# Optimization experiments

Hardware: AMD Instinct MI355X
Metric: run time of the kernel (lower is better)

## Reference

```python
import jax, jax.numpy as jnp
import numpy as np

B, C, H, W = 2, 32, 128, 128
P = 32                      # encoder patch size (== decoder_out_feat_size_final_linear -> empty up_tail)
D = 512                     # encoder dim == decoder dim (enc_to_dec = Identity)
HEADS, DHEAD = 8, 64
ENC_DEPTH = 4
FLIN, CUP = 32, 4
DI, DS, K, DTR, OUTCH = 32, 8, 4, 2, 20   # SS2D dims (c_in=32 hardcoded in module)


def _ln(x, g, b):
    m = x.mean(-1, keepdims=True)
    v = ((x - m) ** 2).mean(-1, keepdims=True)
    return (x - m) / jnp.sqrt(v + 1e-5) * g + b


def _attn(x, g, b, wqkv, wo, bo):
    Bb, N, _ = x.shape
    qkv = _ln(x, g, b) @ wqkv
    q, k, v = jnp.split(qkv, 3, axis=-1)
    sp = lambda t: t.reshape(Bb, N, HEADS, DHEAD).transpose(0, 2, 1, 3)
    q, k, v = sp(q), sp(k), sp(v)
    a = jax.nn.softmax(jnp.einsum('bhnd,bhmd->bhnm', q, k) * (DHEAD ** -0.5), axis=-1)
    o = jnp.einsum('bhnm,bhmd->bhnd', a, v).transpose(0, 2, 1, 3).reshape(Bb, N, HEADS * DHEAD)
    return o @ wo + bo


def _ff(x, g, b, w1, b1, w2, b2):
    return jax.nn.gelu(_ln(x, g, b) @ w1 + b1, approximate=False) @ w2 + b2


def _conv(x, w, b, groups=1):
    y = jax.lax.conv_general_dilated(x, w, (1, 1), 'SAME',
        dimension_numbers=('NCHW', 'OIHW', 'NCHW'), feature_group_count=groups)
    return y + b[None, :, None, None]


def _fft2c(x):
    x = jnp.fft.ifftshift(x, axes=(-2, -1))
    x = jnp.fft.fft2(x, axes=(-2, -1), norm='ortho')
    return jnp.fft.fftshift(x, axes=(-2, -1))


def _ifft2c(x):
    x = jnp.fft.ifftshift(x, axes=(-2, -1))
    x = jnp.fft.ifft2(x, axes=(-2, -1), norm='ortho')
    return jnp.fft.fftshift(x, axes=(-2, -1))


def setup_inputs():
    key = jax.random.key(0)
    it = iter(jax.random.split(key, 80))
    nk = lambda: next(it)
    rn = lambda shape, s=0.02: jax.random.normal(nk(), shape, jnp.float32) * s
    nh, nw = H // P, W // P
    N = nh * nw
    pd = P * P * C
    inp = {}
    inp['in_imgs'] = jax.random.normal(nk(), (B, C, H, W), jnp.float32)
    inp['in_ksp'] = rn((B, C, H, W), 0.01)
    inp['mask'] = (jax.random.uniform(nk(), (B, 1, H, W)) < 0.3).astype(jnp.float32)
    s = jax.random.normal(nk(), (B, C, H, W), jnp.float32)
    sc = s[:, 0::2] + 1j * s[:, 1::2]
    sc = sc / jnp.sqrt(jnp.sum(jnp.abs(sc) ** 2, axis=1, keepdims=True) + 1e-8)
    inp['sens'] = jnp.stack([sc.real, sc.imag], axis=2).reshape(B, C, H, W)
    # patch embedding: LayerNorm(pd) -> Linear(pd, D) -> LayerNorm(D)
    inp['pe_ln1_g'] = jnp.ones((pd,)); inp['pe_ln1_b'] = jnp.zeros((pd,))
    inp['pe_w'] = rn((pd, D)); inp['pe_b'] = jnp.zeros((D,))
    inp['pe_ln2_g'] = jnp.ones((D,)); inp['pe_ln2_b'] = jnp.zeros((D,))
    inp['pos_emb'] = rn((1, N, D))
    dep = ENC_DEPTH
    inp['enc_aln_g'] = jnp.ones((dep, D)); inp['enc_aln_b'] = jnp.zeros((dep, D))
    inp['enc_wqkv'] = rn((dep, D, 3 * HEADS * DHEAD)); inp['enc_wo'] = rn((dep, HEADS * DHEAD, D)); inp['enc_bo'] = jnp.zeros((dep, D))
    inp['enc_fln_g'] = jnp.ones((dep, D)); inp['enc_fln_b'] = jnp.zeros((dep, D))
    inp['enc_w1'] = rn((dep, D, 2048)); inp['enc_b1'] = jnp.zeros((dep, 2048))
    inp['enc_w2'] = rn((dep, 2048, D)); inp['enc_b2'] = jnp.zeros((dep, D))
    inp['enc_ng'] = jnp.ones((D,)); inp['enc_nb'] = jnp.zeros((D,))
    inp['dec_pos'] = rn((N, D))
    inp['dec_aln_g'] = jnp.ones((D,)); inp['dec_aln_b'] = jnp.zeros((D,))
    inp['dec_wqkv'] = rn((D, 3 * HEADS * DHEAD)); inp['dec_wo'] = rn((HEADS * DHEAD, D)); inp['dec_bo'] = jnp.zeros((D,))
    inp['dec_fln_g'] = jnp.ones((D,)); inp['dec_fln_b'] = jnp.zeros((D,))
    inp['dec_w1'] = rn((D, 3072)); inp['dec_b1'] = jnp.zeros((3072,))
    inp['dec_w2'] = rn((3072, D)); inp['dec_b2'] = jnp.zeros((D,))
    inp['dec_ng'] = jnp.ones((D,)); inp['dec_nb'] = jnp.zeros((D,))
    inp['fin_w'] = rn((D, CUP * FLIN * FLIN)); inp['fin_b'] = jnp.zeros((CUP * FLIN * FLIN,))
    # SS2D params
    inp['ss_in_w'] = rn((C, 2 * DI), 0.1); inp['ss_in_b'] = jnp.zeros((2 * DI,))
    inp['ss_conv_w'] = rn((DI, 1, 3, 3), 0.1); inp['ss_conv_b'] = jnp.zeros((DI,))
    inp['ss_xproj'] = rn((K, DI, DTR + 2 * DS), 0.1)
    inp['ss_dt_w'] = rn((K, DTR, DI), 0.5); inp['ss_dt_b'] = rn((K, DI), 0.1)
    inp['ss_Alog'] = jnp.log(jnp.tile(jnp.arange(1, DS + 1, dtype=jnp.float32), (K, DI, 1)))
    inp['ss_D'] = jnp.ones((K, DI))
    inp['ss_ln_g'] = jnp.ones((DI,)); inp['ss_ln_b'] = jnp.zeros((DI,))
    inp['ss_out_w'] = rn((DI, OUTCH), 0.1); inp['ss_out_b'] = jnp.zeros((OUTCH,))
    # RefinementBlock (in_ch = CUP + 32 + OUTCH = 56)
    inp['last_head_w'] = rn((64, CUP + C + OUTCH, 3, 3), 0.05); inp['last_head_b'] = jnp.zeros((64,))
    inp['res_w1'] = rn((3, 64, 64, 3, 3), 0.05); inp['res_b1'] = jnp.zeros((3, 64))
    inp['res_w2'] = rn((3, 64, 64, 3, 3), 0.05); inp['res_b2'] = jnp.zeros((3, 64))
    inp['last_tail_w'] = rn((2, 64, 3, 3), 0.05); inp['last_tail_b'] = jnp.zeros((2,))
    inp['dc_alpha'] = jnp.array(1.0, jnp.float32)
    return inp


def _forward(in_imgs, in_ksp, mask, sens, pe_ln1_g, pe_ln1_b, pe_w, pe_b, pe_ln2_g, pe_ln2_b, pos_emb, enc_aln_g, enc_aln_b, enc_wqkv, enc_wo, enc_bo, enc_fln_g, enc_fln_b, enc_w1, enc_b1, enc_w2, enc_b2, enc_ng, enc_nb, dec_pos, dec_aln_g, dec_aln_b, dec_wqkv, dec_wo, dec_bo, dec_fln_g, dec_fln_b, dec_w1, dec_b1, dec_w2, dec_b2, dec_ng, dec_nb, fin_w, fin_b, ss_in_w, ss_in_b, ss_conv_w, ss_conv_b, ss_xproj, ss_dt_w, ss_dt_b, ss_Alog, ss_D, ss_ln_g, ss_ln_b, ss_out_w, ss_out_b, last_head_w, last_head_b, res_w1, res_b1, res_w2, res_b2, last_tail_w, last_tail_b, dc_alpha):
    nh, nw = H // P, W // P
    N = nh * nw
    # patchify: bb cc (h p1) (w p2) -> bb (h w) (p1 p2 cc)
    pch = in_imgs.reshape(B, C, nh, P, nw, P).transpose(0, 2, 4, 3, 5, 1).reshape(B, N, P * P * C)
    t = _ln(pch, pe_ln1_g, pe_ln1_b) @ pe_w + pe_b
    t = _ln(t, pe_ln2_g, pe_ln2_b)
    t = t + pos_emb   # pool == 'mean'
    for i in range(ENC_DEPTH):
        t = _attn(t, enc_aln_g[i], enc_aln_b[i], enc_wqkv[i], enc_wo[i], enc_bo[i]) + t
        t = _ff(t, enc_fln_g[i], enc_fln_b[i], enc_w1[i], enc_b1[i], enc_w2[i], enc_b2[i]) + t
    t = _ln(t, enc_ng, enc_nb)
    # decoder transformer (depth 1); enc_to_dec is Identity
    d = t + dec_pos[None]
    d = _attn(d, dec_aln_g, dec_aln_b, dec_wqkv, dec_wo, dec_bo) + d
    d = _ff(d, dec_fln_g, dec_fln_b, dec_w1, dec_b1, dec_w2, dec_b2) + d
    d = _ln(d, dec_ng, dec_nb)
    lat = d @ fin_w + fin_b
    # bb (nh nw) (cc p1 p2) -> bb cc (nh p1) (nw p2); up_tail is empty (P == FLIN)
    x = lat.reshape(B, nh, nw, CUP, FLIN, FLIN).transpose(0, 3, 1, 4, 2, 5).reshape(B, CUP, H, W)
    # ---- SS2D: 4-directional selective scan over in_ksp ----
    L = H * W
    xz = jnp.einsum('bchw,ce->behw', in_ksp, ss_in_w) + ss_in_b[None, :, None, None]
    xs0, z = xz[:, :DI], xz[:, DI:]
    xs0 = jax.nn.silu(_conv(xs0, ss_conv_w, ss_conv_b, groups=DI))
    x_hw = xs0.reshape(B, DI, L)
    x_wh = xs0.transpose(0, 1, 3, 2).reshape(B, DI, L)
    xs = jnp.stack([x_hw, x_wh, x_hw[..., ::-1], x_wh[..., ::-1]], axis=1)   # (B,K,DI,L)
    dbl = jnp.einsum('bkdl,kdc->bkcl', xs, ss_xproj)
    dtr, Bm, Cm = dbl[:, :, :DTR], dbl[:, :, DTR:DTR + DS], dbl[:, :, DTR + DS:]
    dts = jax.nn.softplus(jnp.einsum('bkrl,krd->bkdl', dtr, ss_dt_w) + ss_dt_b[None, :, :, None])
    A = -jnp.exp(ss_Alog)
    a = jnp.exp(jnp.einsum('bkdl,kds->bklds', dts, A))         # transition per step
    bb = jnp.einsum('bkdl,bksl->bklds', dts * xs, Bm)          # input per step
    def comb(e1, e2):
        a1, b1 = e1; a2, b2 = e2
        return a1 * a2, a2 * b1 + b2
    _, hs = jax.lax.associative_scan(comb, (a, bb), axis=2)    # (B,K,L,DI,DS)
    ys = jnp.einsum('bklds,bksl->bkdl', hs, Cm) + ss_D[None, :, :, None] * xs
    yh = ys[:, 0] + ys[:, 2, :, ::-1]
    yw = ys[:, 1] + ys[:, 3, :, ::-1]
    y = yh + yw.reshape(B, DI, W, H).transpose(0, 1, 3, 2).reshape(B, DI, L)
    y = y.reshape(B, DI, H, W).transpose(0, 2, 3, 1)           # BHWC
    y = _ln(y, ss_ln_g, ss_ln_b) * jax.nn.silu(z.transpose(0, 2, 3, 1))
    out_ss = (y @ ss_out_w + ss_out_b).transpose(0, 3, 1, 2)   # (B,OUTCH,H,W)
    # ---- refinement ----
    lrelu = lambda v: jnp.where(v > 0, v, 0.2 * v)
    xc = jnp.concatenate([x, in_imgs, out_ss], axis=1)
    h0 = lrelu(_conv(xc, last_head_w, last_head_b))
    for i in range(3):
        h0 = lrelu(h0 + _conv(lrelu(_conv(h0, res_w1[i], res_b1[i])), res_w2[i], res_b2[i]))
    x_ri = _conv(h0, last_tail_w, last_tail_b)   # (B,2,H,W)
    # ---- data consistency ----
    x_c = (x_ri[:, 0] + 1j * x_ri[:, 1])[:, None]
    k_meas = (in_ksp[:, 0::2] + 1j * in_ksp[:, 1::2]) * 100.0   # k_scale_ratio
    s_c = sens[:, 0::2] + 1j * sens[:, 1::2]
    k_pred = _fft2c(s_c * x_c)
    k_dc = k_pred + mask * dc_alpha * (k_meas - k_pred)
    x_comb = jnp.sum(_ifft2c(k_dc) * jnp.conj(s_c), axis=1)
    out_ri = jnp.stack([x_comb.real, x_comb.imag], axis=1)
    return jnp.sqrt(out_ri[:, 0:1] ** 2 + out_ri[:, 1:2] ** 2 + 1e-12)


reference = _forward
```

## Files before the change

### kernel.cpp

```cpp
#include <hip/hip_runtime.h>

#define PI_F 3.14159265358979323846f

constexpr int L_ = 16384;
constexpr int PD_ = 32768;

__device__ __forceinline__ float sigmoidf_(float x){ return 1.f/(1.f+__expf(-x)); }
__device__ __forceinline__ float softplusf_(float x){ return x>20.f ? x : log1pf(__expf(x)); }
__device__ __forceinline__ float geluf_(float x){ return 0.5f*x*(1.f+erff(x*0.70710678118654752f)); }

__device__ __forceinline__ float2 block_reduce2(float s, float ss){
  __shared__ float r1[256], r2[256];
  int tid = threadIdx.x;
  r1[tid]=s; r2[tid]=ss; __syncthreads();
  for(int o=128;o>0;o>>=1){ if(tid<o){ r1[tid]+=r1[tid+o]; r2[tid]+=r2[tid+o]; } __syncthreads(); }
  float2 out; out.x=r1[0]; out.y=r2[0]; __syncthreads();
  return out;
}

__global__ __launch_bounds__(256) void k_pesum(const float* __restrict__ img, float* __restrict__ stats){
  int blk=blockIdx.x; int m=blk>>3, sl=blk&7;
  int b=m>>4, n=m&15, ih=n>>2, iw=n&3;
  int tid=threadIdx.x;
  const float* base=img+(size_t)b*32*L_;
  float s=0.f, ss=0.f;
  for (int i=tid;i<4096;i+=256){
    int j=sl*4096+i;
    int c=j>>10, p1=(j>>5)&31, p2=j&31;
    float v=base[(size_t)c*L_+(ih*32+p1)*128+iw*32+p2];
    s+=v; ss+=v*v;
  }
  float2 r=block_reduce2(s,ss);
  if (tid==0){ atomicAdd(&stats[m*2],r.x); atomicAdd(&stats[m*2+1],r.y); }
}

__global__ __launch_bounds__(256) void k_penorm(const float* __restrict__ img, const float* __restrict__ stats,
                                                const float* __restrict__ g, const float* __restrict__ bv,
                                                float* __restrict__ xn){
  int blk=blockIdx.x; int m=blk>>3, sl=blk&7;
  int b=m>>4, n=m&15, ih=n>>2, iw=n&3;
  int tid=threadIdx.x;
  const float* base=img+(size_t)b*32*L_;
  float mean=stats[m*2]/(float)PD_;
  float var =stats[m*2+1]/(float)PD_-mean*mean;
  float inv =1.f/sqrtf(var+1e-5f);
  for (int i=tid;i<4096;i+=256){
    int j=sl*4096+i;
    int c=j>>10, p1=(j>>5)&31, p2=j&31;
    float v=base[(size_t)c*L_+(ih*32+p1)*128+iw*32+p2];
    int k=(p1*32+p2)*32+c;
    xn[(size_t)m*PD_+k]=(v-mean)*inv*g[k]+bv[k];
  }
}

template<int KC, int MODE>
__global__ __launch_bounds__(256) void k_gemm_sk(const float* __restrict__ A, const float* __restrict__ Bw,
                                                 const float* __restrict__ bias, float* __restrict__ C,
                                                 int N, int K){
  __shared__ float As[32][KC];
  int tid=threadIdx.x, tx=tid&63, ty=tid>>6;
  int n = blockIdx.x*64+tx;
  int k0 = blockIdx.y*KC;
  for (int i=tid;i<32*KC;i+=256){
    int r=i/KC, c=i%KC;
    float v=A[(size_t)r*K + k0 + c];
    if (MODE==1) v=geluf_(v);
    As[r][c]=v;
  }
  __syncthreads();
  float acc[8]={0,0,0,0,0,0,0,0};
  for (int kk=0;kk<KC;kk+=4){
    float b0=Bw[(size_t)(k0+kk)*N+n],   b1=Bw[(size_t)(k0+kk+1)*N+n];
    float b2=Bw[(size_t)(k0+kk+2)*N+n], b3=Bw[(size_t)(k0+kk+3)*N+n];
    #pragma unroll
    for (int r=0;r<8;r++){
      const float4 a=*(const float4*)&As[ty*8+r][kk];
      acc[r]+=a.x*b0+a.y*b1+a.z*b2+a.w*b3;
    }
  }
  bool addb = (bias!=nullptr) && (blockIdx.y==0);
  #pragma unroll
  for (int r=0;r<8;r++){
    int m=ty*8+r;
    float v=acc[r]+(addb?bias[n]:0.f);
    if (MODE==2){
      int b=m>>4, ih=(m>>2)&3, iw=m&3;
      int cu=n>>10, f1=(n>>5)&31, f2=n&31;
      atomicAdd(&C[((size_t)(b*4+cu)*128+ih*32+f1)*128+iw*32+f2], v);
    } else {
      atomicAdd(&C[(size_t)m*N+n], v);
    }
  }
}

__global__ __launch_bounds__(256) void k_pe_post(float* __restrict__ t,
                                                 const float* __restrict__ g, const float* __restrict__ bv,
                                                 const float* __restrict__ pos){
  int m=blockIdx.x, tid=threadIdx.x;
  float v0 = t[m*512+tid];
  float v1 = t[m*512+256+tid];
  float2 r = block_reduce2(v0+v1, v0*v0+v1*v1);
  float mean=r.x/512.f, var=r.y/512.f-mean*mean, inv=1.f/sqrtf(var+1e-5f);
  int n = m&15;
  t[m*512+tid]     = (v0-mean)*inv*g[tid]+bv[tid]         + pos[n*512+tid];
  t[m*512+256+tid] = (v1-mean)*inv*g[256+tid]+bv[256+tid] + pos[n*512+256+tid];
}

__global__ __launch_bounds__(256) void k_ln_tok(const float* __restrict__ src, const float* __restrict__ g,
                                                const float* __restrict__ bv, float* __restrict__ dst){
  int m=blockIdx.x, tid=threadIdx.x;
  float v0=src[m*512+tid], v1=src[m*512+256+tid];
  float2 r=block_reduce2(v0+v1, v0*v0+v1*v1);
  float mean=r.x/512.f, var=r.y/512.f-mean*mean, inv=1.f/sqrtf(var+1e-5f);
  dst[m*512+tid]     =(v0-mean)*inv*g[tid]+bv[tid];
  dst[m*512+256+tid] =(v1-mean)*inv*g[256+tid]+bv[256+tid];
}

__global__ void k_addpos(const float* __restrict__ t, const float* __restrict__ pos, float* __restrict__ dst){
  int i = blockIdx.x*256+threadIdx.x;
  int m=i>>9, j=i&511;
  dst[i]=t[i]+pos[(m&15)*512+j];
}

__global__ __launch_bounds__(256) void k_attn(const float* __restrict__ qkv, float* __restrict__ outb){
  int bh=blockIdx.x, b=bh>>3, h=bh&7, tid=threadIdx.x;
  __shared__ float q[16][64], kk[16][64], vv[16][64], pp[16][16];
  for (int i=tid;i<1024;i+=256){
    int row=i>>6, d=i&63;
    const float* src=qkv + (size_t)(b*16+row)*1536 + h*64+d;
    q[row][d]=src[0]; kk[row][d]=src[512]; vv[row][d]=src[1024];
  }
  __syncthreads();
  int i=tid>>4, j=tid&15;
  float s=0.f;
  #pragma unroll
  for (int d=0;d<64;d++) s+=q[i][d]*kk[j][d];
  s*=0.125f;
  float mx=s;
  for (int o=8;o>0;o>>=1) mx=fmaxf(mx,__shfl_xor(mx,o,16));
  float e=__expf(s-mx), sm=e;
  for (int o=8;o>0;o>>=1) sm+=__shfl_xor(sm,o,16);
  pp[i][j]=e/sm;
  __syncthreads();
  int d=tid&63;
  for (int pass=0;pass<4;pass++){
    int row=pass*4+(tid>>6);
    float acc=0.f;
    #pragma unroll
    for (int jj=0;jj<16;jj++) acc+=pp[row][jj]*vv[jj][d];
    outb[(size_t)(b*16+row)*512 + h*64+d]=acc;
  }
}

__global__ __launch_bounds__(256) void k_xz(const float* __restrict__ ksp, const float* __restrict__ w,
                                            const float* __restrict__ bv, float* __restrict__ xz){
  int blk=blockIdx.x; int b=blk>>6; int p0=(blk&63)*256; int tid=threadIdx.x;
  __shared__ float lin[32][256];
  __shared__ float lw[2048];
  for (int i=tid;i<2048;i+=256) lw[i]=w[i];
  for (int i=tid;i<8192;i+=256){ int c=i>>8, p=i&255; lin[c][p]=ksp[(size_t)(b*32+c)*L_+p0+p]; }
  __syncthreads();
  float xv[32];
  #pragma unroll
  for (int c=0;c<32;c++) xv[c]=lin[c][tid];
  for (int e=0;e<64;e++){
    float a=bv[e];
    #pragma unroll
    for (int c=0;c<32;c++) a+=xv[c]*lw[c*64+e];
    xz[(size_t)(b*64+e)*L_+p0+tid]=a;
  }
}

__global__ void k_dwconv(const float* __restrict__ xz, const float* __restrict__ w,
                         const float* __restrict__ bv, float* __restrict__ xs0){
  int i=blockIdx.x*256+threadIdx.x;
  int p=i&16383; int d=(i>>14)&31; int b=i>>19;
  int h=p>>7, ww=p&127;
  const float* src=xz+(size_t)(b*64+d)*L_;
  float acc=bv[d];
  for (int ky=0;ky<3;ky++){
    int hh=h+ky-1; if(hh<0||hh>127) continue;
    for (int kx=0;kx<3;kx++){
      int wx=ww+kx-1; if(wx<0||wx>127) continue;
      acc+=src[hh*128+wx]*w[d*9+ky*3+kx];
    }
  }
  xs0[(size_t)(b*32+d)*L_+p]=acc*sigmoidf_(acc);
}

__global__ __launch_bounds__(256) void k_transpose(const float* __restrict__ src, float* __restrict__ dst){
  __shared__ float tile[32][33];
  int z=blockIdx.z;
  int h0=blockIdx.y*32, w0=blockIdx.x*32;
  int tid=threadIdx.x, tx=tid&31, ty=tid>>5;
  const float* s=src+(size_t)z*L_;
  float* d=dst+(size_t)z*L_;
  for (int r=ty;r<32;r+=8) tile[r][tx]=s[(h0+r)*128+w0+tx];
  __syncthreads();
  for (int r=ty;r<32;r+=8) d[(w0+r)*128+h0+tx]=tile[tx][r];
}

__global__ __launch_bounds__(256) void k_dbl(const float* __restrict__ xs0, const float* __restrict__ xs0T,
                                             const float* __restrict__ xproj, float* __restrict__ dbl){
  int bk=blockIdx.y; int b=bk>>2, k=bk&3;
  int l0=blockIdx.x*256, tid=threadIdx.x;
  const float* src=(k&1)?xs0T:xs0;
  __shared__ float xv[32][256];
  __shared__ float xp[576];
  for (int i=tid;i<576;i+=256) xp[i]=xproj[k*576+i];
  for (int i=tid;i<8192;i+=256){
    int dd=i>>8, p=i&255; int l=l0+p; int li=(k<2)?l:(16383-l);
    xv[dd][p]=src[(size_t)(b*32+dd)*L_+li];
  }
  __syncthreads();
  float xr[32];
  #pragma unroll
  for (int dd=0;dd<32;dd++) xr[dd]=xv[dd][tid];
  float* out=&dbl[((size_t)(b*4+k)*L_ + l0+tid)*18];
  for (int c=0;c<18;c++){
    float a=0.f;
    #pragma unroll
    for (int dd=0;dd<32;dd++) a+=xr[dd]*xp[dd*18+c];
    out[c]=a;
  }
}

__global__ __launch_bounds__(256) void k_scan1(const float* __restrict__ dbl, const float* __restrict__ xs0,
                                               const float* __restrict__ xs0T, const float* __restrict__ dtw,
                                               const float* __restrict__ dtb, const float* __restrict__ Alog,
                                               float2* __restrict__ sm){
  int blk=blockIdx.x; int bk=blk>>7, c=blk&127;
  int b=bk>>2, k=bk&3;
  int tid=threadIdx.x, d=tid>>3, s=tid&7;
  __shared__ float ed[128][18];
  __shared__ float xsl[32][128];
  const float* dbase=dbl+((size_t)bk*L_+c*128)*18;
  for (int i=tid;i<2304;i+=256) ((float*)ed)[i]=dbase[i];
  const float* src=(k&1)?xs0T:xs0;
  bool rev=(k>=2);
  for (int i=tid;i<4096;i+=256){
    int dd=i>>7, j=i&127; int l=c*128+j;
    xsl[dd][j]=src[(size_t)(b*32+dd)*L_+(rev?(16383-l):l)];
  }
  __syncthreads();
  float w0=dtw[(k*2+0)*32+d], w1=dtw[(k*2+1)*32+d], bb=dtb[k*32+d];
  float Av=-__expf(Alog[(k*32+d)*8+s]);
  float P=1.f, Q=0.f;
  for (int j=0;j<128;j++){
    float dt=softplusf_(ed[j][0]*w0+ed[j][1]*w1+bb);
    float u=dt*xsl[d][j];
    float a=__expf(dt*Av);
    Q=a*Q+u*ed[j][2+s];
    P*=a;
  }
  sm[((size_t)bk*128+c)*256+tid]=make_float2(P,Q);
}

__global__ __launch_bounds__(256) void k_scan2(const float2* __restrict__ sm, float* __restrict__ pre){
  int bk=blockIdx.x, tid=threadIdx.x;
  float run=0.f;
  for (int c=0;c<128;c++){
    size_t idx=((size_t)bk*128+c)*256+tid;
    pre[idx]=run;
    float2 pq=sm[idx];
    run=pq.x*run+pq.y;
  }
}

__global__ __launch_bounds__(256) void k_scan3(const float* __restrict__ dbl, const float* __restrict__ xs0,
                                               const float* __restrict__ xs0T, const float* __restrict__ dtw,
                                               const float* __restrict__ dtb, const float* __restrict__ Alog,
                                               const float* __restrict__ Dp, const float* __restrict__ pre,
                                               float* __restrict__ ys){
  int blk=blockIdx.x; int bk=blk>>7, c=blk&127;
  int b=bk>>2, k=bk&3;
  int tid=threadIdx.x, d=tid>>3, s=tid&7;
  __shared__ float ed[128][18];
  __shared__ float xsl[32][128];
  __shared__ float ybuf[32][128];
  const float* dbase=dbl+((size_t)bk*L_+c*128)*18;
  for (int i=tid;i<2304;i+=256) ((float*)ed)[i]=dbase[i];
  const float* src=(k&1)?xs0T:xs0;
  bool rev=(k>=2);
  for (int i=tid;i<4096;i+=256){
    int dd=i>>7, j=i&127; int l=c*128+j;
    xsl[dd][j]=src[(size_t)(b*32+dd)*L_+(rev?(16383-l):l)];
  }
  __syncthreads();
  float w0=dtw[(k*2+0)*32+d], w1=dtw[(k*2+1)*32+d], bb=dtb[k*32+d];
  float Av=-__expf(Alog[(k*32+d)*8+s]);
  float Dv=Dp[k*32+d];
  float h=pre[((size_t)bk*128+c)*256+tid];
  for (int j=0;j<128;j++){
    float xsv=xsl[d][j];
    float dt=softplusf_(ed[j][0]*w0+ed[j][1]*w1+bb);
    float u=dt*xsv;
    float a=__expf(dt*Av);
    h=a*h+u*ed[j][2+s];
    float yp=h*ed[j][10+s];
    yp+=__shfl_xor(yp,1,8);
    yp+=__shfl_xor(yp,2,8);
    yp+=__shfl_xor(yp,4,8);
    if (s==0) ybuf[d][j]=yp+Dv*xsv;
  }
  __syncthreads();
  float* yout=ys+((size_t)bk*32)*L_+c*128;
  for (int i=tid;i<4096;i+=256){
    int dd=i>>7, j=i&127;
    yout[(size_t)dd*L_+j]=ybuf[dd][j];
  }
}

__global__ __launch_bounds__(256) void k_ycomb(const float* __restrict__ ys, const float* __restrict__ xz,
                                               const float* __restrict__ g, const float* __restrict__ bv,
                                               const float* __restrict__ ow, const float* __restrict__ ob,
                                               float* __restrict__ oss){
  int blk=blockIdx.x; int b=blk>>6; int p=(blk&63)*256+threadIdx.x;
  int h=p>>7, w=p&127; int lt=w*128+h;
  __shared__ float lw[640]; __shared__ float lb[20]; __shared__ float lg[32], lbv[32];
  int tid=threadIdx.x;
  for (int i=tid;i<640;i+=256) lw[i]=ow[i];
  if (tid<20) lb[tid]=ob[tid];
  if (tid<32){ lg[tid]=g[tid]; lbv[tid]=bv[tid]; }
  __syncthreads();
  size_t base=(size_t)b*4*32*L_;
  float y[32];
  float s=0.f, ss=0.f;
  #pragma unroll
  for (int d=0;d<32;d++){
    float v=ys[base+(size_t)(0*32+d)*L_+p] + ys[base+(size_t)(2*32+d)*L_+16383-p]
          + ys[base+(size_t)(1*32+d)*L_+lt] + ys[base+(size_t)(3*32+d)*L_+16383-lt];
    y[d]=v; s+=v; ss+=v*v;
  }
  float mean=s/32.f, var=ss/32.f-mean*mean, inv=1.f/sqrtf(var+1e-5f);
  #pragma unroll
  for (int d=0;d<32;d++){
    float yn=(y[d]-mean)*inv*lg[d]+lbv[d];
    float zv=xz[(size_t)(b*64+32+d)*L_+p];
    y[d]=yn*(zv*sigmoidf_(zv));
  }
  for (int c=0;c<20;c++){
    float a=lb[c];
    #pragma unroll
    for (int d=0;d<32;d++) a+=y[d]*lw[d*20+c];
    oss[(size_t)(b*20+c)*L_+p]=a;
  }
}

__global__ void k_concat(const float* __restrict__ x, const float* __restrict__ img,
                         const float* __restrict__ oss, float* __restrict__ xc){
  int i=blockIdx.x*256+threadIdx.x;
  int p=i&16383; int ch=(i>>14)%56; int b=i/(56*16384);
  float v;
  if (ch<4) v=x[(size_t)(b*4+ch)*L_+p];
  else if (ch<36) v=img[(size_t)(b*32+ch-4)*L_+p];
  else v=oss[(size_t)(b*20+ch-36)*L_+p];
  xc[i]=v;
}

template<int NCO>
__global__ __launch_bounds__(256) void k_conv3s(const float* __restrict__ in, const float* __restrict__ wt,
                                                float* __restrict__ sc, int Cin, int Cout, int CIS){
  int tile=blockIdx.x; int th0=(tile>>2)*32, tw0=(tile&3)*32;
  int cg=blockIdx.y;
  int bz=blockIdx.z; int b=bz>>1, ks=bz&1;
  int cibase=ks*CIS;
  int cic=Cin-cibase; if (cic>CIS) cic=CIS;
  __shared__ float wlds[32][NCO][9];
  __shared__ float ibuf[2][34][34];
  int tid=threadIdx.x;
  for (int i=tid;i<cic*NCO*9;i+=256){
    int ci=i/(NCO*9), rem=i%(NCO*9), co=rem/9, q=rem%9;
    wlds[ci][co][q]=wt[(((size_t)(cg*NCO+co))*Cin + cibase+ci)*9+q];
  }
  auto stage=[&](int buf, int ci){
    const float* src=in+((size_t)b*Cin+cibase+ci)*L_;
    for (int i=tid;i<34*34;i+=256){
      int r=i/34, c=i%34;
      int gh=th0+r-1, gw=tw0+c-1;
      ibuf[buf][r][c]=(gh>=0&&gh<128&&gw>=0&&gw<128)?src[gh*128+gw]:0.f;
    }
  };
  stage(0,0);
  __syncthreads();
  float acc[NCO][4];
  #pragma unroll
  for (int co=0;co<NCO;co++){acc[co][0]=0.f;acc[co][1]=0.f;acc[co][2]=0.f;acc[co][3]=0.f;}
  int tr=((tid>>4)&15)<<1, tc=(tid&15)<<1;
  for (int ci=0;ci<cic;ci++){
    int cur=ci&1;
    if (ci+1<cic) stage(cur^1, ci+1);
    float iv[4][4];
    #pragma unroll
    for (int dr=0;dr<4;dr++)
      #pragma unroll
      for (int dc=0;dc<4;dc++) iv[dr][dc]=ibuf[cur][tr+dr][tc+dc];
    #pragma unroll
    for (int co=0;co<NCO;co++){
      float w0=wlds[ci][co][0],w1=wlds[ci][co][1],w2=wlds[ci][co][2];
      float w3=wlds[ci][co][3],w4=wlds[ci][co][4],w5=wlds[ci][co][5];
      float w6=wlds[ci][co][6],w7=wlds[ci][co][7],w8=wlds[ci][co][8];
      acc[co][0]+=iv[0][0]*w0+iv[0][1]*w1+iv[0][2]*w2
                 +iv[1][0]*w3+iv[1][1]*w4+iv[1][2]*w5
                 +iv[2][0]*w6+iv[2][1]*w7+iv[2][2]*w8;
      acc[co][1]+=iv[0][1]*w0+iv[0][2]*w1+iv[0][3]*w2
                 +iv[1][1]*w3+iv[1][2]*w4+iv[1][3]*w5
                 +iv[2][1]*w6+iv[2][2]*w7+iv[2][3]*w8;
      acc[co][2]+=iv[1][0]*w0+iv[1][1]*w1+iv[1][2]*w2
                 +iv[2][0]*w3+iv[2][1]*w4+iv[2][2]*w5
                 +iv[3][0]*w6+iv[3][1]*w7+iv[3][2]*w8;
      acc[co][3]+=iv[1][1]*w0+iv[1][2]*w1+iv[1][3]*w2
                 +iv[2][1]*w3+iv[2][2]*w4+iv[2][3]*w5
                 +iv[3][1]*w6+iv[3][2]*w7+iv[3][3]*w8;
    }
    __syncthreads();
  }
  #pragma unroll
  for (int co=0;co<NCO;co++){
    int gco=cg*NCO+co;
    float* dst=sc+((size_t)((ks*2+b)*Cout+gco))*L_+(size_t)(th0+tr)*128+tw0+tc;
    float2 a={acc[co][0],acc[co][1]}, c={acc[co][2],acc[co][3]};
    *(float2*)dst=a;
    *(float2*)(dst+128)=c;
  }
}

__global__ void k_epi(const float* __restrict__ sc, const float* __restrict__ bias,
                      const float* __restrict__ res, float* __restrict__ out, int Cout, int act){
  int i=blockIdx.x*256+threadIdx.x;
  int co=(i/L_)%Cout;
  size_t half=(size_t)2*Cout*L_;
  float v=sc[i]+sc[half+i]+bias[co];
  if (res) v+=res[i];
  if (act) v=v>0.f?v:0.2f*v;
  out[i]=v;
}

__device__ __forceinline__ int rev7(int x){
  return ((x&1)<<6)|((x&2)<<4)|((x&4)<<2)|(x&8)|((x&16)>>2)|((x&32)>>4)|((x&64)>>6);
}

__global__ __launch_bounds__(256) void k_fftA(const float* __restrict__ x_ri, const float* __restrict__ sens,
                                              float* __restrict__ tmp){
  int blk=blockIdx.x; int b=blk>>7, coil=(blk>>3)&15, rg=blk&7;
  int r0=rg*16;
  __shared__ float Ar[16][128], Ai[16][128];
  __shared__ float twr[64], twi[64];
  int tid=threadIdx.x;
  if (tid<64){ float ang=-2.f*PI_F*(float)tid/128.f; twr[tid]=cosf(ang); twi[tid]=sinf(ang); }
  const float* srp=sens+(size_t)(b*32+2*coil)*L_;
  const float* sip=sens+(size_t)(b*32+2*coil+1)*L_;
  const float* xrp=x_ri+(size_t)(b*2)*L_;
  const float* xip=xrp+L_;
  for (int i=tid;i<2048;i+=256){
    int lr=i>>7, w=i&127; int gh=r0+lr; int idx=gh*128+w;
    float sg=((gh+w)&1)?-1.f:1.f;
    float sr=srp[idx],si=sip[idx],xr=xrp[idx],xi=xip[idx];
    Ar[lr][w]=sg*(sr*xr-si*xi);
    Ai[lr][w]=sg*(sr*xi+si*xr);
  }
  __syncthreads();
  for (int s=0;s<7;s++){
    int m=64>>s;
    for (int q=tid;q<1024;q+=256){
      int lr=q>>6, jj=q&63;
      int j=jj&(m-1), gg=jj>>(6-s);
      int kpos=(gg<<(7-s))+j;
      int tw=j<<s;
      float ur=Ar[lr][kpos],ui=Ai[lr][kpos],vr=Ar[lr][kpos+m],vi=Ai[lr][kpos+m];
      Ar[lr][kpos]=ur+vr; Ai[lr][kpos]=ui+vi;
      float dr=ur-vr,di=ui-vi,wr=twr[tw],wi=twi[tw];
      Ar[lr][kpos+m]=dr*wr-di*wi; Ai[lr][kpos+m]=dr*wi+di*wr;
    }
    __syncthreads();
  }
  float* tr=tmp+(size_t)(b*16+coil)*2*L_;
  float* ti=tr+L_;
  for (int i=tid;i<2048;i+=256){
    int lr=i>>7, w=i&127; int idx=(r0+lr)*128+w;
    tr[idx]=Ar[lr][w]; ti[idx]=Ai[lr][w];
  }
}

__global__ __launch_bounds__(256) void k_fftB(float* __restrict__ tmp, const float* __restrict__ ksp,
                                              const float* __restrict__ mask, const float* __restrict__ alpha_p){
  int blk=blockIdx.x; int b=blk>>7, coil=(blk>>3)&15, cg=blk&7;
  int c0=cg*16;
  __shared__ float Br[128][17], Bi[128][17];
  __shared__ float twr[64], twi[64];
  int tid=threadIdx.x;
  if (tid<64){ float ang=-2.f*PI_F*(float)tid/128.f; twr[tid]=cosf(ang); twi[tid]=sinf(ang); }
  float* tr=tmp+(size_t)(b*16+coil)*2*L_;
  float* ti=tr+L_;
  for (int i=tid;i<2048;i+=256){
    int r=i>>4, lc=i&15;
    Br[r][lc]=tr[r*128+c0+lc]; Bi[r][lc]=ti[r*128+c0+lc];
  }
  __syncthreads();
  for (int s=0;s<7;s++){
    int m=64>>s;
    for (int q=tid;q<1024;q+=256){
      int lc=q&15, jj=q>>4;
      int j=jj&(m-1), gg=jj>>(6-s);
      int kpos=(gg<<(7-s))+j;
      int tw=j<<s;
      float ur=Br[kpos][lc],ui=Bi[kpos][lc],vr=Br[kpos+m][lc],vi=Bi[kpos+m][lc];
      Br[kpos][lc]=ur+vr; Bi[kpos][lc]=ui+vi;
      float dr=ur-vr,di=ui-vi,wr=twr[tw],wi=twi[tw];
      Br[kpos+m][lc]=dr*wr-di*wi; Bi[kpos+m][lc]=dr*wi+di*wr;
    }
    __syncthreads();
  }
  float alpha=alpha_p[0];
  const float* krp=ksp+(size_t)(b*32+2*coil)*L_;
  const float* kip=ksp+(size_t)(b*32+2*coil+1)*L_;
  const float* mkp=mask+(size_t)b*L_;
  for (int i=tid;i<2048;i+=256){
    int r=i>>4, lc=i&15;
    int k1=rev7(r), k2=rev7(c0+lc);
    int kidx=k1*128+k2;
    float mv=mkp[kidx]*alpha;
    float sg=((k1+k2)&1)?-128.f:128.f;
    float kr=krp[kidx]*100.f*sg, ki=kip[kidx]*100.f*sg;
    Br[r][lc]=(1.f-mv)*Br[r][lc]+mv*kr;
    Bi[r][lc]=(1.f-mv)*Bi[r][lc]+mv*ki;
  }
  __syncthreads();
  for (int s=0;s<7;s++){
    int m=1<<s;
    for (int q=tid;q<1024;q+=256){
      int lc=q&15, jj=q>>4;
      int j=jj&(m-1), gg=jj>>s;
      int kpos=(gg<<(s+1))+j;
      int tw=j<<(6-s);
      float wr=twr[tw], wi=-twi[tw];
      float vr=Br[kpos+m][lc],vi=Bi[kpos+m][lc];
      float t2r=vr*wr-vi*wi, t2i=vr*wi+vi*wr;
      float ur=Br[kpos][lc],ui=Bi[kpos][lc];
      Br[kpos][lc]=ur+t2r; Bi[kpos][lc]=ui+t2i;
      Br[kpos+m][lc]=ur-t2r; Bi[kpos+m][lc]=ui-t2i;
    }
    __syncthreads();
  }
  for (int i=tid;i<2048;i+=256){
    int r=i>>4, lc=i&15;
    tr[r*128+c0+lc]=Br[r][lc]; ti[r*128+c0+lc]=Bi[r][lc];
  }
}

__global__ __launch_bounds__(256) void k_fftC(const float* __restrict__ tmp, const float* __restrict__ sens,
                                              float* __restrict__ acc){
  int blk=blockIdx.x; int b=blk>>7, coil=(blk>>3)&15, rg=blk&7;
  int r0=rg*16;
  __shared__ float Ar[16][128], Ai[16][128];
  __shared__ float twr[64], twi[64];
  int tid=threadIdx.x;
  if (tid<64){ float ang=-2.f*PI_F*(float)tid/128.f; twr[tid]=cosf(ang); twi[tid]=sinf(ang); }
  const float* tr=tmp+(size_t)(b*16+coil)*2*L_;
  const float* ti=tr+L_;
  for (int i=tid;i<2048;i+=256){
    int lr=i>>7, w=i&127; int idx=(r0+lr)*128+w;
    Ar[lr][w]=tr[idx]; Ai[lr][w]=ti[idx];
  }
  __syncthreads();
  for (int s=0;s<7;s++){
    int m=1<<s;
    for (int q=tid;q<1024;q+=256){
      int lr=q>>6, jj=q&63;
      int j=jj&(m-1), gg=jj>>s;
      int kpos=(gg<<(s+1))+j;
      int tw=j<<(6-s);
      float wr=twr[tw], wi=-twi[tw];
      float vr=Ar[lr][kpos+m],vi=Ai[lr][kpos+m];
      float t2r=vr*wr-vi*wi, t2i=vr*wi+vi*wr;
      float ur=Ar[lr][kpos],ui=Ai[lr][kpos];
      Ar[lr][kpos]=ur+t2r; Ai[lr][kpos]=ui+t2i;
      Ar[lr][kpos+m]=ur-t2r; Ai[lr][kpos+m]=ui-t2i;
    }
    __syncthreads();
  }
  const float* srp=sens+(size_t)(b*32+2*coil)*L_;
  const float* sip=sens+(size_t)(b*32+2*coil+1)*L_;
  float* accr=acc+(size_t)(b*2)*L_;
  float* acci=accr+L_;
  for (int i=tid;i<2048;i+=256){
    int lr=i>>7, w=i&127; int gh=r0+lr; int idx=gh*128+w;
    float sc=(((gh+w)&1)?-1.f:1.f)*(1.f/16384.f);
    float wr2=Ar[lr][w]*sc, wi2=Ai[lr][w]*sc;
    float sr=srp[idx], si=sip[idx];
    atomicAdd(&accr[idx], sr*wr2+si*wi2);
    atomicAdd(&acci[idx], sr*wi2-si*wr2);
  }
}

__global__ void k_mag(const float* __restrict__ acc, float* __restrict__ out){
  int i=blockIdx.x*256+threadIdx.x;
  int b=i>>14, p=i&16383;
  float re=acc[(size_t)(b*2)*L_+p], im=acc[(size_t)(b*2+1)*L_+p];
  out[i]=sqrtf(re*re+im*im+1e-12f);
}

extern "C" void kernel_launch(void* const* d_in, const int* in_sizes, int n_in,
                              void* d_out, int out_size, void* d_ws, size_t ws_size,
                              hipStream_t stream){
  const float* in_imgs=(const float*)d_in[0];
  const float* in_ksp=(const float*)d_in[1];
  const float* mask=(const float*)d_in[2];
  const float* sens=(const float*)d_in[3];
  const float* pe_ln1_g=(const float*)d_in[4];
  const float* pe_ln1_b=(const float*)d_in[5];
  const float* pe_w=(const float*)d_in[6];
  const float* pe_b=(const float*)d_in[7];
  const float* pe_ln2_g=(const float*)d_in[8];
  const float* pe_ln2_b=(const float*)d_in[9];
  const float* pos_emb=(const float*)d_in[10];
  const float* enc_aln_g=(const float*)d_in[11];
  const float* enc_aln_b=(const float*)d_in[12];
  const float* enc_wqkv=(const float*)d_in[13];
  const float* enc_wo=(const float*)d_in[14];
  const float* enc_bo=(const float*)d_in[15];
  const float* enc_fln_g=(const float*)d_in[16];
  const float* enc_fln_b=(const float*)d_in[17];
  const float* enc_w1=(const float*)d_in[18];
  const float* enc_b1=(const float*)d_in[19];
  const float* enc_w2=(const float*)d_in[20];
  const float* enc_b2=(const float*)d_in[21];
  const float* enc_ng=(const float*)d_in[22];
  const float* enc_nb=(const float*)d_in[23];
  const float* dec_pos=(const float*)d_in[24];
  const float* dec_aln_g=(const float*)d_in[25];
  const float* dec_aln_b=(const float*)d_in[26];
  const float* dec_wqkv=(const float*)d_in[27];
  const float* dec_wo=(const float*)d_in[28];
  const float* dec_bo=(const float*)d_in[29];
  const float* dec_fln_g=(const float*)d_in[30];
  const float* dec_fln_b=(const float*)d_in[31];
  const float* dec_w1=(const float*)d_in[32];
  const float* dec_b1=(const float*)d_in[33];
  const float* dec_w2=(const float*)d_in[34];
  const float* dec_b2=(const float*)d_in[35];
  const float* dec_ng=(const float*)d_in[36];
  const float* dec_nb=(const float*)d_in[37];
  const float* fin_w=(const float*)d_in[38];
  const float* fin_b=(const float*)d_in[39];
  const float* ss_in_w=(const float*)d_in[40];
  const float* ss_in_b=(const float*)d_in[41];
  const float* ss_conv_w=(const float*)d_in[42];
  const float* ss_conv_b=(const float*)d_in[43];
  const float* ss_xproj=(const float*)d_in[44];
  const float* ss_dt_w=(const float*)d_in[45];
  const float* ss_dt_b=(const float*)d_in[46];
  const float* ss_Alog=(const float*)d_in[47];
  const float* ss_D=(const float*)d_in[48];
  const float* ss_ln_g=(const float*)d_in[49];
  const float* ss_ln_b=(const float*)d_in[50];
  const float* ss_out_w=(const float*)d_in[51];
  const float* ss_out_b=(const float*)d_in[52];
  const float* head_w=(const float*)d_in[53];
  const float* head_b=(const float*)d_in[54];
  const float* res_w1=(const float*)d_in[55];
  const float* res_b1=(const float*)d_in[56];
  const float* res_w2=(const float*)d_in[57];
  const float* res_b2=(const float*)d_in[58];
  const float* tail_w=(const float*)d_in[59];
  const float* tail_b=(const float*)d_in[60];
  const float* dc_alpha=(const float*)d_in[61];

  char* ws=(char*)d_ws;
  size_t off=0;
  auto alloc=[&](size_t nfloats)->float*{ float* p=(float*)(ws+off); off+=((nfloats*4+255)/256)*256; return p; };
  float* xn   =alloc((size_t)32*32768);
  float* stats=alloc(64);
  float* tA   =alloc(32*512);
  float* tB   =alloc(32*512);
  float* aln  =alloc(32*512);
  float* qkv  =alloc(32*1536);
  float* attno=alloc(32*512);
  float* ffh  =alloc(32*3072);
  float* xup  =alloc((size_t)2*4*L_);
  float* xz   =alloc((size_t)2*64*L_);
  float* xs0  =alloc((size_t)2*32*L_);
  float* xs0T =alloc((size_t)2*32*L_);
  float* dbl  =alloc((size_t)2*4*L_*18);
  float* ys   =alloc((size_t)2*4*32*L_);
  float* smv  =alloc((size_t)8*128*256*2);
  float* prев =alloc((size_t)8*128*256);
  float* oss  =alloc((size_t)2*20*L_);
  float* xc   =alloc((size_t)2*56*L_);
  float* h0   =alloc((size_t)2*64*L_);
  float* tmpc =alloc((size_t)2*64*L_);
  float* csc  =alloc((size_t)2*2*64*L_);
  float* x_ri =alloc((size_t)2*2*L_);
  float* ftmp =alloc((size_t)32*2*L_);
  float* accb =alloc((size_t)2*2*L_);
  (void)ws_size; (void)in_sizes; (void)n_in; (void)out_size;

  hipMemsetAsync(stats, 0, 64*4, stream);
  k_pesum<<<256,256,0,stream>>>(in_imgs, stats);
  k_penorm<<<256,256,0,stream>>>(in_imgs, stats, pe_ln1_g, pe_ln1_b, xn);
  hipMemsetAsync(tA, 0, 32*512*4, stream);
  k_gemm_sk<256,0><<<dim3(8,128),256,0,stream>>>(xn, pe_w, pe_b, tA, 512, 32768);
  k_pe_post<<<32,256,0,stream>>>(tA, pe_ln2_g, pe_ln2_b, pos_emb);

  for (int i=0;i<4;i++){
    k_ln_tok<<<32,256,0,stream>>>(tA, enc_aln_g+i*512, enc_aln_b+i*512, aln);
    hipMemsetAsync(qkv, 0, 32*1536*4, stream);
    k_gemm_sk<64,0><<<dim3(24,8),256,0,stream>>>(aln, enc_wqkv+(size_t)i*512*1536, nullptr, qkv, 1536, 512);
    k_attn<<<16,256,0,stream>>>(qkv, attno);
    k_gemm_sk<64,0><<<dim3(8,8),256,0,stream>>>(attno, enc_wo+(size_t)i*512*512, enc_bo+i*512, tA, 512, 512);
    k_ln_tok<<<32,256,0,stream>>>(tA, enc_fln_g+i*512, enc_fln_b+i*512, aln);
    hipMemsetAsync(ffh, 0, 32*2048*4, stream);
    k_gemm_sk<64,0><<<dim3(32,8),256,0,stream>>>(aln, enc_w1+(size_t)i*512*2048, enc_b1+i*2048, ffh, 2048, 512);
    k_gemm_sk<64,1><<<dim3(8,32),256,0,stream>>>(ffh, enc_w2+(size_t)i*2048*512, enc_b2+i*512, tA, 512, 2048);
  }
  k_ln_tok<<<32,256,0,stream>>>(tA, enc_ng, enc_nb, tA);
  k_addpos<<<64,256,0,stream>>>(tA, dec_pos, tB);
  k_ln_tok<<<32,256,0,stream>>>(tB, dec_aln_g, dec_aln_b, aln);
  hipMemsetAsync(qkv, 0, 32*1536*4, stream);
  k_gemm_sk<64,0><<<dim3(24,8),256,0,stream>>>(aln, dec_wqkv, nullptr, qkv, 1536, 512);
  k_attn<<<16,256,0,stream>>>(qkv, attno);
  k_gemm_sk<64,0><<<dim3(8,8),256,0,stream>>>(attno, dec_wo, dec_bo, tB, 512, 512);
  k_ln_tok<<<32,256,0,stream>>>(tB, dec_fln_g, dec_fln_b, aln);
  hipMemsetAsync(ffh, 0, 32*3072*4, stream);
  k_gemm_sk<64,0><<<dim3(48,8),256,0,stream>>>(aln, dec_w1, dec_b1, ffh, 3072, 512);
  k_gemm_sk<64,1><<<dim3(8,48),256,0,stream>>>(ffh, dec_w2, dec_b2, tB, 512, 3072);
  k_ln_tok<<<32,256,0,stream>>>(tB, dec_ng, dec_nb, tB);
  hipMemsetAsync(xup, 0, (size_t)2*4*L_*4, stream);
  k_gemm_sk<64,2><<<dim3(64,8),256,0,stream>>>(tB, fin_w, fin_b, xup, 4096, 512);

  k_xz<<<128,256,0,stream>>>(in_ksp, ss_in_w, ss_in_b, xz);
  k_dwconv<<<4096,256,0,stream>>>(xz, ss_conv_w, ss_conv_b, xs0);
  k_transpose<<<dim3(4,4,64),256,0,stream>>>(xs0, xs0T);
  k_dbl<<<dim3(64,8),256,0,stream>>>(xs0, xs0T, ss_xproj, dbl);
  k_scan1<<<1024,256,0,stream>>>(dbl, xs0, xs0T, ss_dt_w, ss_dt_b, ss_Alog, (float2*)smv);
  k_scan2<<<8,256,0,stream>>>((const float2*)smv, prев);
  k_scan3<<<1024,256,0,stream>>>(dbl, xs0, xs0T, ss_dt_w, ss_dt_b, ss_Alog, ss_D, prев, ys);
  k_ycomb<<<128,256,0,stream>>>(ys, xz, ss_ln_g, ss_ln_b, ss_out_w, ss_out_b, oss);

  k_concat<<<7168,256,0,stream>>>(xup, in_imgs, oss, xc);
  k_conv3s<4><<<dim3(16,16,4),256,0,stream>>>(xc, head_w, csc, 56, 64, 28);
  k_epi<<<8192,256,0,stream>>>(csc, head_b, nullptr, h0, 64, 1);
  for (int i=0;i<3;i++){
    k_conv3s<4><<<dim3(16,16,4),256,0,stream>>>(h0, res_w1+(size_t)i*64*64*9, csc, 64, 64, 32);
    k_epi<<<8192,256,0,stream>>>(csc, res_b1+i*64, nullptr, tmpc, 64, 1);
    k_conv3s<4><<<dim3(16,16,4),256,0,stream>>>(tmpc, res_w2+(size_t)i*64*64*9, csc, 64, 64, 32);
    k_epi<<<8192,256,0,stream>>>(csc, res_b2+i*64, h0, h0, 64, 1);
  }
  k_conv3s<2><<<dim3(16,1,4),256,0,stream>>>(h0, tail_w, csc, 64, 2, 32);
  k_epi<<<256,256,0,stream>>>(csc, tail_b, nullptr, x_ri, 2, 0);

  hipMemsetAsync(accb, 0, (size_t)2*2*L_*4, stream);
  k_fftA<<<256,256,0,stream>>>(x_ri, sens, ftmp);
  k_fftB<<<256,256,0,stream>>>(ftmp, in_ksp, mask, dc_alpha);
  k_fftC<<<256,256,0,stream>>>(ftmp, sens, accb);
  k_mag<<<128,256,0,stream>>>(accb, (float*)d_out);
}
```

Baseline: 1.792 ms.

## Precompute dt and dt*x per chunk in shared memory and restructure SS2D combine

```diff
diff --git a/kernel.cpp b/kernel.cpp
--- a/kernel.cpp
+++ b/kernel.cpp
@@ -233,24 +233,26 @@
   int b=bk>>2, k=bk&3;
   int tid=threadIdx.x, d=tid>>3, s=tid&7;
   __shared__ float ed[128][18];
-  __shared__ float xsl[32][128];
+  __shared__ float2 du[32][129];
   const float* dbase=dbl+((size_t)bk*L_+c*128)*18;
   for (int i=tid;i<2304;i+=256) ((float*)ed)[i]=dbase[i];
+  __syncthreads();
   const float* src=(k&1)?xs0T:xs0;
   bool rev=(k>=2);
   for (int i=tid;i<4096;i+=256){
     int dd=i>>7, j=i&127; int l=c*128+j;
-    xsl[dd][j]=src[(size_t)(b*32+dd)*L_+(rev?(16383-l):l)];
-  }
-  __syncthreads();
-  float w0=dtw[(k*2+0)*32+d], w1=dtw[(k*2+1)*32+d], bb=dtb[k*32+d];
+    float xsv=src[(size_t)(b*32+dd)*L_+(rev?(16383-l):l)];
+    float w0=dtw[(k*2+0)*32+dd], w1=dtw[(k*2+1)*32+dd], bb=dtb[k*32+dd];
+    float dt=softplusf_(ed[j][0]*w0+ed[j][1]*w1+bb);
+    du[dd][j]=make_float2(dt, dt*xsv);
+  }
+  __syncthreads();
   float Av=-__expf(Alog[(k*32+d)*8+s]);
   float P=1.f, Q=0.f;
   for (int j=0;j<128;j++){
-    float dt=softplusf_(ed[j][0]*w0+ed[j][1]*w1+bb);
-    float u=dt*xsl[d][j];
-    float a=__expf(dt*Av);
-    Q=a*Q+u*ed[j][2+s];
+    float2 v=du[d][j];
+    float a=__expf(v.x*Av);
+    Q=a*Q+v.y*ed[j][2+s];
     P*=a;
   }
   sm[((size_t)bk*128+c)*256+tid]=make_float2(P,Q);
@@ -259,91 +261,108 @@
 __global__ __launch_bounds__(256) void k_scan2(const float2* __restrict__ sm, float* __restrict__ pre){
   int bk=blockIdx.x, tid=threadIdx.x;
   float run=0.f;
-  for (int c=0;c<128;c++){
-    size_t idx=((size_t)bk*128+c)*256+tid;
-    pre[idx]=run;
-    float2 pq=sm[idx];
-    run=pq.x*run+pq.y;
+  for (int cb=0; cb<128; cb+=16){
+    float2 v[16];
+    #pragma unroll
+    for (int t=0;t<16;t++) v[t]=sm[((size_t)bk*128+cb+t)*256+tid];
+    #pragma unroll
+    for (int t=0;t<16;t++){
+      pre[((size_t)bk*128+cb+t)*256+tid]=run;
+      run=v[t].x*run+v[t].y;
+    }
   }
 }
 
 __global__ __launch_bounds__(256) void k_scan3(const float* __restrict__ dbl, const float* __restrict__ xs0,
                                                const float* __restrict__ xs0T, const float* __restrict__ dtw,
                                                const float* __restrict__ dtb, const float* __restrict__ Alog,
-                                               const float* __restrict__ Dp, const float* __restrict__ pre,
-                                               float* __restrict__ ys){
+                                               const float* __restrict__ pre, float* __restrict__ ys){
   int blk=blockIdx.x; int bk=blk>>7, c=blk&127;
   int b=bk>>2, k=bk&3;
   int tid=threadIdx.x, d=tid>>3, s=tid&7;
   __shared__ float ed[128][18];
-  __shared__ float xsl[32][128];
-  __shared__ float ybuf[32][128];
+  __shared__ float2 du[32][129];
   const float* dbase=dbl+((size_t)bk*L_+c*128)*18;
   for (int i=tid;i<2304;i+=256) ((float*)ed)[i]=dbase[i];
+  __syncthreads();
   const float* src=(k&1)?xs0T:xs0;
   bool rev=(k>=2);
   for (int i=tid;i<4096;i+=256){
     int dd=i>>7, j=i&127; int l=c*128+j;
-    xsl[dd][j]=src[(size_t)(b*32+dd)*L_+(rev?(16383-l):l)];
-  }
-  __syncthreads();
-  float w0=dtw[(k*2+0)*32+d], w1=dtw[(k*2+1)*32+d], bb=dtb[k*32+d];
+    float xsv=src[(size_t)(b*32+dd)*L_+(rev?(16383-l):l)];
+    float w0=dtw[(k*2+0)*32+dd], w1=dtw[(k*2+1)*32+dd], bb=dtb[k*32+dd];
+    float dt=softplusf_(ed[j][0]*w0+ed[j][1]*w1+bb);
+    du[dd][j]=make_float2(dt, dt*xsv);
+  }
+  __syncthreads();
   float Av=-__expf(Alog[(k*32+d)*8+s]);
-  float Dv=Dp[k*32+d];
   float h=pre[((size_t)bk*128+c)*256+tid];
+  float* yout=ys+((size_t)bk*32+d)*L_+c*128;
   for (int j=0;j<128;j++){
-    float xsv=xsl[d][j];
-    float dt=softplusf_(ed[j][0]*w0+ed[j][1]*w1+bb);
-    float u=dt*xsv;
-    float a=__expf(dt*Av);
-    h=a*h+u*ed[j][2+s];
+    float2 v=du[d][j];
+    float a=__expf(v.x*Av);
+    h=a*h+v.y*ed[j][2+s];
     float yp=h*ed[j][10+s];
     yp+=__shfl_xor(yp,1,8);
     yp+=__shfl_xor(yp,2,8);
     yp+=__shfl_xor(yp,4,8);
-    if (s==0) ybuf[d][j]=yp+Dv*xsv;
-  }
-  __syncthreads();
-  float* yout=ys+((size_t)bk*32)*L_+c*128;
-  for (int i=tid;i<4096;i+=256){
-    int dd=i>>7, j=i&127;
-    yout[(size_t)dd*L_+j]=ybuf[dd][j];
+    if (s==0) yout[j]=yp;
   }
 }
 
 __global__ __launch_bounds__(256) void k_ycomb(const float* __restrict__ ys, const float* __restrict__ xz,
+                                               const float* __restrict__ xs0, const float* __restrict__ Dp,
                                                const float* __restrict__ g, const float* __restrict__ bv,
                                                const float* __restrict__ ow, const float* __restrict__ ob,
                                                float* __restrict__ oss){
-  int blk=blockIdx.x; int b=blk>>6; int p=(blk&63)*256+threadIdx.x;
-  int h=p>>7, w=p&127; int lt=w*128+h;
-  __shared__ float lw[640]; __shared__ float lb[20]; __shared__ float lg[32], lbv[32];
-  int tid=threadIdx.x;
+  int blk=blockIdx.x; int b=blk>>7; int pg=blk&127;
+  int tid=threadIdx.x; int pos=tid&127; int team=tid>>7;
+  int p=pg*128+pos;
+  int lt=pos*128+pg;
+  __shared__ float lw[640]; __shared__ float lb[20]; __shared__ float lg[32], lbv[32], lD[32];
+  __shared__ float red[2][2][128];
+  __shared__ float prj[128][21];
   for (int i=tid;i<640;i+=256) lw[i]=ow[i];
   if (tid<20) lb[tid]=ob[tid];
-  if (tid<32){ lg[tid]=g[tid]; lbv[tid]=bv[tid]; }
-  __syncthreads();
-  size_t base=(size_t)b*4*32*L_;
-  float y[32];
+  if (tid<32){ lg[tid]=g[tid]; lbv[tid]=bv[tid]; lD[tid]=Dp[tid]+Dp[32+tid]+Dp[64+tid]+Dp[96+tid]; }
+  __syncthreads();
+  size_t base=(size_t)b*128*L_;
+  int d0=team*16;
+  float y[16];
   float s=0.f, ss=0.f;
   #pragma unroll
-  for (int d=0;d<32;d++){
+  for (int dd=0;dd<16;dd++){
+    int d=d0+dd;
     float v=ys[base+(size_t)(0*32+d)*L_+p] + ys[base+(size_t)(2*32+d)*L_+16383-p]
-          + ys[base+(size_t)(1*32+d)*L_+lt] + ys[base+(size_t)(3*32+d)*L_+16383-lt];
-    y[d]=v; s+=v; ss+=v*v;
-  }
-  float mean=s/32.f, var=ss/32.f-mean*mean, inv=1.f/sqrtf(var+1e-5f);
-  #pragma unroll
-  for (int d=0;d<32;d++){
-    float yn=(y[d]-mean)*inv*lg[d]+lbv[d];
+          + ys[base+(size_t)(1*32+d)*L_+lt] + ys[base+(size_t)(3*32+d)*L_+16383-lt]
+          + lD[d]*xs0[(size_t)(b*32+d)*L_+p];
+    y[dd]=v; s+=v; ss+=v*v;
+  }
+  red[team][0][pos]=s; red[team][1][pos]=ss;
+  __syncthreads();
+  float S=red[0][0][pos]+red[1][0][pos];
+  float SS=red[0][1][pos]+red[1][1][pos];
+  float mean=S/32.f, var=SS/32.f-mean*mean, inv=1.f/sqrtf(var+1e-5f);
+  float pc[20];
+  #pragma unroll
+  for (int c2=0;c2<20;c2++) pc[c2]=0.f;
+  #pragma unroll
+  for (int dd=0;dd<16;dd++){
+    int d=d0+dd;
+    float yn=(y[dd]-mean)*inv*lg[d]+lbv[d];
     float zv=xz[(size_t)(b*64+32+d)*L_+p];
-    y[d]=yn*(zv*sigmoidf_(zv));
-  }
-  for (int c=0;c<20;c++){
-    float a=lb[c];
-    #pragma unroll
-    for (int d=0;d<32;d++) a+=y[d]*lw[d*20+c];
-    oss[(size_t)(b*20+c)*L_+p]=a;
+    float t2=yn*(zv*sigmoidf_(zv));
+    #pragma unroll
+    for (int c2=0;c2<20;c2++) pc[c2]+=t2*lw[d*20+c2];
+  }
+  if (team==1){
+    #pragma unroll
+    for (int c2=0;c2<20;c2++) prj[pos][c2]=pc[c2];
+  }
+  __syncthreads();
+  if (team==0){
+    #pragma unroll
+    for (int c2=0;c2<20;c2++) oss[(size_t)(b*20+c2)*L_+p]=lb[c2]+pc[c2]+prj[pos][c2];
   }
 }
 
@@ -684,7 +703,7 @@
   float* dbl  =alloc((size_t)2*4*L_*18);
   float* ys   =alloc((size_t)2*4*32*L_);
   float* smv  =alloc((size_t)8*128*256*2);
-  float* prев =alloc((size_t)8*128*256);
+  float* prebuf=alloc((size_t)8*128*256);
   float* oss  =alloc((size_t)2*20*L_);
   float* xc   =alloc((size_t)2*56*L_);
   float* h0   =alloc((size_t)2*64*L_);
@@ -733,9 +752,9 @@
   k_transpose<<<dim3(4,4,64),256,0,stream>>>(xs0, xs0T);
   k_dbl<<<dim3(64,8),256,0,stream>>>(xs0, xs0T, ss_xproj, dbl);
   k_scan1<<<1024,256,0,stream>>>(dbl, xs0, xs0T, ss_dt_w, ss_dt_b, ss_Alog, (float2*)smv);
-  k_scan2<<<8,256,0,stream>>>((const float2*)smv, prев);
-  k_scan3<<<1024,256,0,stream>>>(dbl, xs0, xs0T, ss_dt_w, ss_dt_b, ss_Alog, ss_D, prев, ys);
-  k_ycomb<<<128,256,0,stream>>>(ys, xz, ss_ln_g, ss_ln_b, ss_out_w, ss_out_b, oss);
+  k_scan2<<<8,256,0,stream>>>((const float2*)smv, prebuf);
+  k_scan3<<<1024,256,0,stream>>>(dbl, xs0, xs0T, ss_dt_w, ss_dt_b, ss_Alog, prebuf, ys);
+  k_ycomb<<<256,256,0,stream>>>(ys, xz, xs0, ss_D, ss_ln_g, ss_ln_b, ss_out_w, ss_out_b, oss);
 
   k_concat<<<7168,256,0,stream>>>(xup, in_imgs, oss, xc);
   k_conv3s<4><<<dim3(16,16,4),256,0,stream>>>(xc, head_w, csc, 56, 64, 28);
```

New measurement: 1.582 ms. 11.7% less time.
